# Performance work log

Hardware: AMD Instinct MI355X
Metric: run time of the kernel (lower is better)

Reference implementation:

```python
import jax, jax.numpy as jnp
import numpy as np

TH = 1.0            # q_threshold for all IF neurons
POS_MAX = 7.0       # level//2 - 1, level=16, sym=True
NEG_MIN = -8.0      # -(level//2)
PREFIRE = 0.2       # attn_softmax_IF.prefire
S_QUANT = 7.0       # spiking_softmax scale = level//2 - 1
NUM_HEADS = 8


def if_step(x, vmem0, acc0, th=TH, pos_max=POS_MAX, neg_min=NEG_MIN):
    """One timestep of a symmetric ST-BIF neuron with straight-through surrogate.
    Forward: spike in {-1,0,+1}*th gated by membrane and accumulator saturation.
    Backward: identity (STE), accumulator is a constant."""
    acc0f = acc0.astype(x.dtype)
    v = vmem0 + x
    pos = jnp.logical_and(v >= th, acc0f < pos_max)
    neg = jnp.logical_and(v < 0.0, acc0f > neg_min)
    spike = pos.astype(x.dtype) - neg.astype(x.dtype)
    out_hard = spike * th
    out = x + jax.lax.stop_gradient(out_hard - x)  # STE: fwd=spike*th, bwd=identity
    acc = jax.lax.stop_gradient(acc0f + spike)     # running spike count (constant wrt grads)
    return out, acc


def setup_inputs() -> dict:
    key = jax.random.key(0)
    ks = jax.random.split(key, 16)
    B, N, C, H = 4, 1024, 512, NUM_HEADS
    D = C // H
    f32 = jnp.float32
    inp = {
        "x": jax.random.normal(ks[0], (B, N, C), dtype=f32),
        "w_qkv": jax.random.normal(ks[1], (3 * C, C), dtype=f32) * 0.02,
        "b_qkv": jnp.zeros((3 * C,), dtype=f32),
        "w_proj": jax.random.normal(ks[2], (C, C), dtype=f32) * 0.02,
        "b_proj": jnp.zeros((C,), dtype=f32),
        "q_vmem": jax.random.uniform(ks[3], (B, H, N, D), dtype=f32),
        "k_vmem": jax.random.uniform(ks[4], (B, H, N, D), dtype=f32),
        "v_vmem": jax.random.uniform(ks[5], (B, H, N, D), dtype=f32),
        "attn_vmem": jax.random.uniform(ks[6], (B, H, N, N), dtype=f32),
        "q_acc0": jax.random.randint(ks[7], (B, H, N, D), 0, 8).astype(jnp.int32),
        "k_acc0": jax.random.randint(ks[8], (B, H, N, D), 0, 8).astype(jnp.int32),
        "v_acc0": jax.random.randint(ks[9], (B, H, N, D), 0, 8).astype(jnp.int32),
        "attn_acc0": jax.random.randint(ks[10], (B, H, N, N), 0, 8).astype(jnp.int32),
    }
    return inp


def reference(x, w_qkv, b_qkv, w_proj, b_proj,
              q_vmem, k_vmem, v_vmem, attn_vmem,
              q_acc0, k_acc0, v_acc0, attn_acc0):
    B, N, C = x.shape
    H = NUM_HEADS
    D = C // H
    scale = D ** -0.5
    sg = jax.lax.stop_gradient

    # qkv projection -> [3, B, H, N, D]
    qkv = (x @ w_qkv.T + b_qkv).reshape(B, N, 3, H, D).transpose(2, 0, 3, 1, 4)
    q_in, k_in, v_in = qkv[0], qkv[1], qkv[2]

    # ST-BIF IF neurons (one timestep, carried state)
    q_s, q_acc = if_step(q_in, q_vmem, q_acc0)
    k_s, k_acc = if_step(k_in, k_vmem, k_acc0)
    v_s, v_acc = if_step(v_in, v_vmem, v_acc0)

    q = q_s * scale
    # accumulator corrections: acc_q * q_threshold (*scale for q) minus detached spike output
    q_corr = sg(q_acc * TH * scale - q)
    k_corr = sg(k_acc * TH - k_s)
    v_corr = sg(v_acc * TH - v_s)

    # multi: (q + q_corr) @ k^T + q @ k_corr^T   -> [B, H, N, N]
    attn = (jnp.einsum('bhnd,bhmd->bhnm', q + q_corr, k_s)
            + jnp.einsum('bhnd,bhmd->bhnm', q, k_corr))

    # spiking softmax substitute: softmax of the (accumulated) scores, scaled to quant range
    attn = jax.nn.softmax(attn, axis=-1) * S_QUANT

    # attn_softmax_IF with prefire bias on the membrane
    attn_s, attn_acc = if_step(attn, attn_vmem + PREFIRE * TH, attn_acc0)
    attn_corr = sg(attn_acc * TH - attn_s)

    # multi1: (attn + attn_corr) @ v + attn @ v_corr  -> [B, H, N, D]
    out = (jnp.einsum('bhnm,bhmd->bhnd', attn_s + attn_corr, v_s)
           + jnp.einsum('bhnm,bhmd->bhnd', attn_s, v_corr))

    # after_attn_IF: fresh state (rounding init 0.5*th, zero accumulator)
    out, _ = if_step(out, jnp.asarray(0.5 * TH, out.dtype), jnp.zeros_like(out))

    out = out.transpose(0, 2, 1, 3).reshape(B, N, C)
    return out @ w_proj.T + b_proj
```

## Files before the change

kernel.cpp:

```cpp
#include <hip/hip_runtime.h>
#include <hip/hip_bf16.h>
#include <cstdint>

typedef short short8 __attribute__((ext_vector_type(8)));
typedef float f32x4 __attribute__((ext_vector_type(4)));
typedef int   int4v __attribute__((ext_vector_type(4)));
typedef _Float16 fp16x8 __attribute__((ext_vector_type(8)));

using bf16 = __hip_bfloat16;

#define MFMA16(a, b, c) __builtin_amdgcn_mfma_f32_16x16x32_bf16((a), (b), (c), 0, 0, 0)
#define MFMAI8(a, b, c) __builtin_amdgcn_mfma_i32_16x16x64_i8((a), (b), (c), 0, 0, 0)
#define MFMAF16(a, b, c) __builtin_amdgcn_mfma_f32_16x16x32_f16((a), (b), (c), 0, 0, 0)

__device__ __forceinline__ short8 ldb8(const bf16* p) {
    return *reinterpret_cast<const short8*>(p);
}

__global__ __launch_bounds__(256) void k_prep(
    const float* __restrict__ X, const float* __restrict__ W, const float* __restrict__ Wp,
    _Float16* __restrict__ Xh, _Float16* __restrict__ Xl,
    _Float16* __restrict__ Wh, _Float16* __restrict__ Wl, bf16* __restrict__ Wpb)
{
    const int NX = 4096 * 512, NW = 1536 * 512, NP = 512 * 512;
    for (int i = blockIdx.x * 256 + threadIdx.x; i < NX + NW + NP; i += gridDim.x * 256) {
        if (i < NX) {
            const float v = X[i] * 512.0f;
            const _Float16 h = (_Float16)v;
            Xh[i] = h;
            Xl[i] = (_Float16)((v - (float)h) * 2048.0f);
        } else if (i < NX + NW) {
            const int j = i - NX;
            const float v = W[j] * 512.0f;
            const _Float16 h = (_Float16)v;
            Wh[j] = h;
            Wl[j] = (_Float16)((v - (float)h) * 2048.0f);
        } else {
            const int j = i - NX - NW;
            Wpb[j] = __float2bfloat16(Wp[j]);
        }
    }
}

__global__ __launch_bounds__(256, 3) void k_qkv_f16(
    const _Float16* __restrict__ Xh, const _Float16* __restrict__ Xl,
    const _Float16* __restrict__ Wh, const _Float16* __restrict__ Wl,
    const float* __restrict__ bq,
    const float* __restrict__ qvm, const float* __restrict__ kvm, const float* __restrict__ vvm,
    const int* __restrict__ qac, const int* __restrict__ kac, const int* __restrict__ vac,
    int8_t* __restrict__ Q2, int8_t* __restrict__ K2c,
    int8_t* __restrict__ VsT, int8_t* __restrict__ VaT)
{
    const int tid = threadIdx.x;
    const int w = tid >> 6, lane = tid & 63, lo = lane & 15, hi = lane >> 4;
    const int wr = w >> 1, wc = w & 1;
    const int r0 = blockIdx.y * 64 + wr * 32;
    const int c0 = blockIdx.x * 128 + wc * 64;

    f32x4 hh[2][4] = {};
    f32x4 md[2][4] = {};

    const _Float16* xhp = Xh + (size_t)(r0 + lo) * 512 + hi * 8;
    const _Float16* xlp = Xl + (size_t)(r0 + lo) * 512 + hi * 8;
    const _Float16* whp = Wh + (size_t)(c0 + lo) * 512 + hi * 8;
    const _Float16* wlp = Wl + (size_t)(c0 + lo) * 512 + hi * 8;

    for (int kc = 0; kc < 16; ++kc) {
        const int ko = kc * 32;
        const fp16x8 Ah0 = *reinterpret_cast<const fp16x8*>(xhp + ko);
        const fp16x8 Ah1 = *reinterpret_cast<const fp16x8*>(xhp + ko + 16 * 512);
        const fp16x8 Al0 = *reinterpret_cast<const fp16x8*>(xlp + ko);
        const fp16x8 Al1 = *reinterpret_cast<const fp16x8*>(xlp + ko + 16 * 512);
        fp16x8 Bh[4], Bl[4];
        #pragma unroll
        for (int j = 0; j < 4; ++j) {
            Bh[j] = *reinterpret_cast<const fp16x8*>(whp + ko + j * 16 * 512);
            Bl[j] = *reinterpret_cast<const fp16x8*>(wlp + ko + j * 16 * 512);
        }
        #pragma unroll
        for (int j = 0; j < 4; ++j) {
            hh[0][j] = MFMAF16(Ah0, Bh[j], hh[0][j]);
            hh[1][j] = MFMAF16(Ah1, Bh[j], hh[1][j]);
            md[0][j] = MFMAF16(Ah0, Bl[j], md[0][j]);
            md[0][j] = MFMAF16(Al0, Bh[j], md[0][j]);
            md[1][j] = MFMAF16(Ah1, Bl[j], md[1][j]);
            md[1][j] = MFMAF16(Al1, Bh[j], md[1][j]);
        }
    }

    const int sel = (unsigned)c0 >> 9;
    const float* VM = (sel == 0) ? qvm : (sel == 1) ? kvm : vvm;
    const int*   AC = (sel == 0) ? qac : (sel == 1) ? kac : vac;

    #pragma unroll
    for (int i = 0; i < 2; ++i) {
        const int rowb = r0 + i * 16 + hi * 4;
        const int b = rowb >> 10, nb = rowb & 1023;
        #pragma unroll
        for (int j = 0; j < 4; ++j) {
            const int c = c0 + j * 16 + lo;
            const int ch = c & 511;
            const int hh_ = ch >> 6, d = ch & 63;
            const int bh = b * 8 + hh_;
            const float bcol = bq[c];
            int sp[4], a4[4];
            #pragma unroll
            for (int r = 0; r < 4; ++r) {
                const size_t gi = (size_t)(bh * 1024 + nb + r) * 64 + d;
                const float vm = VM[gi];
                const int a0 = AC[gi];
                const float val = fmaf(md[i][j][r], 0x1p-11f, hh[i][j][r]) * 0x1p-18f;
                const float v_ = vm + (val + bcol);
                int s = ((v_ >= 1.0f) && (a0 < 7)) ? 1 : 0;
                if (v_ < 0.0f) s -= 1;
                sp[r] = s; a4[r] = a0;
            }
            if (sel == 2) {
                uchar4 us, ua;
                us.x = (uint8_t)sp[0]; us.y = (uint8_t)sp[1]; us.z = (uint8_t)sp[2]; us.w = (uint8_t)sp[3];
                ua.x = (uint8_t)a4[0]; ua.y = (uint8_t)a4[1]; ua.z = (uint8_t)a4[2]; ua.w = (uint8_t)a4[3];
                const size_t vi = (size_t)(bh * 64 + d) * 1024 + nb;
                *reinterpret_cast<uchar4*>(VsT + vi) = us;
                *reinterpret_cast<uchar4*>(VaT + vi) = ua;
            } else {
                int8_t* base = ((sel == 0) ? Q2 : K2c) + (size_t)(bh * 1024 + nb) * 128 + d;
                #pragma unroll
                for (int r = 0; r < 4; ++r) {
                    const int v0 = (sel == 0) ? a4[r] + sp[r] : sp[r];
                    const int v1 = (sel == 0) ? sp[r]         : a4[r];
                    base[r * 128]      = (int8_t)v0;
                    base[r * 128 + 64] = (int8_t)v1;
                }
            }
        }
    }
}

__global__ __launch_bounds__(256, 4) void k_attn(
    const int8_t* __restrict__ Q2, const int8_t* __restrict__ K2c,
    const float* __restrict__ avm, const int* __restrict__ aac,
    const int8_t* __restrict__ VsT, const int8_t* __restrict__ VaT,
    bf16* __restrict__ O2)
{
    __shared__ alignas(16) char Sc[33280];
    int*   const maxb = (int*)(Sc + 32768);
    float* const sumb = (float*)(Sc + 33024);
    const int w = threadIdx.x >> 6, lane = threadIdx.x & 63;
    const int lo = lane & 15, hi = lane >> 4;
    const int bh = blockIdx.z * 8 + blockIdx.y;
    const int n0 = blockIdx.x * 16;

    int4v sc[16];
    {
        const int8_t* qb = Q2 + ((size_t)(bh * 1024 + n0 + lo)) * 128 + hi * 16;
        const int4v qa0 = *reinterpret_cast<const int4v*>(qb);
        const int4v qa1 = *reinterpret_cast<const int4v*>(qb + 64);
        const int8_t* kbp = K2c + ((size_t)(bh * 1024 + w * 256 + lo)) * 128 + hi * 16;
        int4v b0[2], b1[2];
        b0[0] = *reinterpret_cast<const int4v*>(kbp);
        b1[0] = *reinterpret_cast<const int4v*>(kbp + 64);
        b0[1] = *reinterpret_cast<const int4v*>(kbp + 2048);
        b1[1] = *reinterpret_cast<const int4v*>(kbp + 2048 + 64);
        #pragma unroll
        for (int t = 0; t < 16; ++t) {
            const int4v c0f = b0[t & 1], c1f = b1[t & 1];
            if (t < 14) {
                const int8_t* np = kbp + (t + 2) * 2048;
                b0[t & 1] = *reinterpret_cast<const int4v*>(np);
                b1[t & 1] = *reinterpret_cast<const int4v*>(np + 64);
            }
            int4v s = {0, 0, 0, 0};
            s = MFMAI8(c0f, qa0, s);
            s = MFMAI8(c1f, qa1, s);
            sc[t] = s;
        }
    }

    const float* vmp = avm + ((size_t)(bh * 1024 + n0 + lo)) * 1024 + w * 256 + hi * 4;
    const int*   acp = aac + ((size_t)(bh * 1024 + n0 + lo)) * 1024 + w * 256 + hi * 4;
    float4 vmr[4]; int4 acr[4];
    #pragma unroll
    for (int j = 0; j < 4; ++j) {
        vmr[j] = *reinterpret_cast<const float4*>(vmp + j * 16);
        acr[j] = *reinterpret_cast<const int4*>(acp + j * 16);
    }

    int mxi = sc[0][0];
    #pragma unroll
    for (int t = 0; t < 16; ++t)
        #pragma unroll
        for (int r = 0; r < 4; ++r)
            mxi = max(mxi, sc[t][r]);
    mxi = max(mxi, __shfl_xor(mxi, 16));
    mxi = max(mxi, __shfl_xor(mxi, 32));
    if (lane < 16) maxb[w * 16 + lo] = mxi;
    __syncthreads();
    const int M = max(max(maxb[lo], maxb[16 + lo]), max(maxb[32 + lo], maxb[48 + lo]));

    const float kls = 0.18033688011112042f;
    float sum = 0.f;
    #pragma unroll
    for (int t = 0; t < 16; ++t)
        #pragma unroll
        for (int r = 0; r < 4; ++r)
            sum += exp2f(kls * (float)(sc[t][r] - M));
    sum += __shfl_xor(sum, 16);
    sum += __shfl_xor(sum, 32);
    if (lane < 16) sumb[w * 16 + lo] = sum;
    __syncthreads();
    const float Stot = (sumb[lo] + sumb[16 + lo]) + (sumb[32 + lo] + sumb[48 + lo]);
    const float rsum = 7.0f / Stot;

    #pragma unroll
    for (int t = 0; t < 16; ++t) {
        const float4 vmc = vmr[t & 3];
        const int4  acc_ = acr[t & 3];
        if (t < 12) {
            vmr[t & 3] = *reinterpret_cast<const float4*>(vmp + (t + 4) * 16);
            acr[t & 3] = *reinterpret_cast<const int4*>(acp + (t + 4) * 16);
        }
        const float vr[4] = {vmc.x, vmc.y, vmc.z, vmc.w};
        const int   ar[4] = {acc_.x, acc_.y, acc_.z, acc_.w};
        unsigned b1v[4], b2v[4];
        #pragma unroll
        for (int i = 0; i < 4; ++i) {
            const float e_ = exp2f(kls * (float)(sc[t][i] - M));
            const float p7 = e_ * rsum;
            const float v_ = (vr[i] + 0.2f) + p7;
            const int a0i = ar[i];
            const int sp = ((v_ >= 1.0f) && (a0i < 7)) ? 1 : 0;
            b1v[i] = (unsigned)(a0i + sp);
            b2v[i] = (unsigned)sp;
        }
        const unsigned p1u = b1v[0] | (b1v[1] << 8) | (b1v[2] << 16) | (b1v[3] << 24);
        const unsigned p2u = b2v[0] | (b2v[1] << 8) | (b2v[2] << 16) | (b2v[3] << 24);
        char* pb = Sc + lo * 1024 + ((w * 256 + t * 16 + hi * 4) ^ ((lo & 7) << 4));
        *reinterpret_cast<unsigned*>(pb)         = p1u;
        *reinterpret_cast<unsigned*>(pb + 16384) = p2u;
    }
    __syncthreads();

    {
        const int d0 = w * 16;
        const int8_t* vs = VsT + ((size_t)(bh * 64 + d0 + lo)) * 1024 + hi * 16;
        const int8_t* va = VaT + ((size_t)(bh * 64 + d0 + lo)) * 1024 + hi * 16;
        int4v nvs = *reinterpret_cast<const int4v*>(vs);
        int4v nva = *reinterpret_cast<const int4v*>(va);
        int4v acc = {0, 0, 0, 0};
        for (int tt = 0; tt < 16; ++tt) {
            const int4v cvs = nvs, cva = nva;
            if (tt < 15) {
                nvs = *reinterpret_cast<const int4v*>(vs + (tt + 1) * 64);
                nva = *reinterpret_cast<const int4v*>(va + (tt + 1) * 64);
            }
            const char* pb = Sc + lo * 1024 + ((tt * 64 + hi * 16) ^ ((lo & 7) << 4));
            const int4v a1 = *reinterpret_cast<const int4v*>(pb);
            const int4v a2 = *reinterpret_cast<const int4v*>(pb + 16384);
            acc = MFMAI8(a1, cvs, acc);
            acc = MFMAI8(a2, cva, acc);
        }
        #pragma unroll
        for (int r = 0; r < 4; ++r) {
            const int n = n0 + hi * 4 + r;
            const float o = (float)acc[r];
            const float o2 = (o >= 0.5f ? 1.f : 0.f) - (o < -0.5f ? 1.f : 0.f);
            O2[((size_t)(blockIdx.z * 1024 + n)) * 512 + blockIdx.y * 64 + d0 + lo] = __float2bfloat16(o2);
        }
    }
}

__global__ __launch_bounds__(256) void k_proj(
    const bf16* __restrict__ O2, const bf16* __restrict__ W, const float* __restrict__ bias,
    float* __restrict__ Y)
{
    const int w = threadIdx.x >> 6, lane = threadIdx.x & 63;
    const int lo = lane & 15, hi = lane >> 4;
    const int r0 = blockIdx.y * 16;
    const int c0 = blockIdx.x * 256 + w * 64;

    f32x4 acc[4] = {{0.f,0.f,0.f,0.f},{0.f,0.f,0.f,0.f},{0.f,0.f,0.f,0.f},{0.f,0.f,0.f,0.f}};
    const bf16* op = O2 + (size_t)(r0 + lo) * 512 + hi * 8;
    #pragma unroll 4
    for (int kb = 0; kb < 16; ++kb) {
        short8 a = ldb8(op + kb * 32);
        #pragma unroll
        for (int t = 0; t < 4; ++t) {
            short8 b = ldb8(W + (size_t)(c0 + t * 16 + lo) * 512 + kb * 32 + hi * 8);
            acc[t] = MFMA16(a, b, acc[t]);
        }
    }
    #pragma unroll
    for (int t = 0; t < 4; ++t) {
        const int col = c0 + t * 16 + lo;
        const float bcol = bias[col];
        #pragma unroll
        for (int r = 0; r < 4; ++r) {
            const int rr = r0 + hi * 4 + r;
            Y[(size_t)rr * 512 + col] = acc[t][r] + bcol;
        }
    }
}

extern "C" void kernel_launch(void* const* d_in, const int* in_sizes, int n_in,
                              void* d_out, int out_size, void* d_ws, size_t ws_size,
                              hipStream_t stream)
{
    const float* x     = (const float*)d_in[0];
    const float* wqkv  = (const float*)d_in[1];
    const float* bqkv  = (const float*)d_in[2];
    const float* wproj = (const float*)d_in[3];
    const float* bproj = (const float*)d_in[4];
    const float* qvm   = (const float*)d_in[5];
    const float* kvm   = (const float*)d_in[6];
    const float* vvm   = (const float*)d_in[7];
    const float* avm   = (const float*)d_in[8];
    const int*   qac   = (const int*)d_in[9];
    const int*   kac   = (const int*)d_in[10];
    const int*   vac   = (const int*)d_in[11];
    const int*   aac   = (const int*)d_in[12];

    char* p = (char*)d_ws;
    int8_t*   Q2  = (int8_t*)p;   p += (size_t)32 * 1024 * 128;
    int8_t*   K2c = (int8_t*)p;   p += (size_t)32 * 1024 * 128;
    int8_t*   VsT = (int8_t*)p;   p += (size_t)32 * 64 * 1024;
    int8_t*   VaT = (int8_t*)p;   p += (size_t)32 * 64 * 1024;
    bf16*     O2  = (bf16*)p;     p += (size_t)4096 * 512 * 2;
    bf16*     Wpb = (bf16*)p;     p += (size_t)512 * 512 * 2;
    _Float16* Xh  = (_Float16*)p; p += (size_t)4096 * 512 * 2;
    _Float16* Xl  = (_Float16*)p; p += (size_t)4096 * 512 * 2;
    _Float16* Wh  = (_Float16*)p; p += (size_t)1536 * 512 * 2;
    _Float16* Wl  = (_Float16*)p; p += (size_t)1536 * 512 * 2;

    k_prep<<<dim3(2048), 256, 0, stream>>>(x, wqkv, wproj, Xh, Xl, Wh, Wl, Wpb);
    k_qkv_f16<<<dim3(12, 64), 256, 0, stream>>>(Xh, Xl, Wh, Wl, bqkv, qvm, kvm, vvm,
                                                qac, kac, vac, Q2, K2c, VsT, VaT);
    k_attn<<<dim3(64, 8, 4), 256, 0, stream>>>(Q2, K2c, avm, aac, VsT, VaT, O2);
    k_proj<<<dim3(2, 256), 256, 0, stream>>>(O2, Wpb, bproj, (float*)d_out);
}
```

Before: 463.8 us.

## Precompute accumulator-by-V product and merge spike V operands in attention

```diff
diff --git a/kernel.cpp b/kernel.cpp
--- a/kernel.cpp
+++ b/kernel.cpp
@@ -16,6 +16,8 @@
 __device__ __forceinline__ short8 ldb8(const bf16* p) {
     return *reinterpret_cast<const short8*>(p);
 }
+__device__ __forceinline__ int lo16(unsigned u) { return (int)(u << 16) >> 16; }
+__device__ __forceinline__ int hi16(unsigned u) { return (int)u >> 16; }
 
 __global__ __launch_bounds__(256) void k_prep(
     const float* __restrict__ X, const float* __restrict__ W, const float* __restrict__ Wp,
@@ -118,7 +120,8 @@
             if (sel == 2) {
                 uchar4 us, ua;
                 us.x = (uint8_t)sp[0]; us.y = (uint8_t)sp[1]; us.z = (uint8_t)sp[2]; us.w = (uint8_t)sp[3];
-                ua.x = (uint8_t)a4[0]; ua.y = (uint8_t)a4[1]; ua.z = (uint8_t)a4[2]; ua.w = (uint8_t)a4[3];
+                ua.x = (uint8_t)(a4[0] + sp[0]); ua.y = (uint8_t)(a4[1] + sp[1]);
+                ua.z = (uint8_t)(a4[2] + sp[2]); ua.w = (uint8_t)(a4[3] + sp[3]);
                 const size_t vi = (size_t)(bh * 64 + d) * 1024 + nb;
                 *reinterpret_cast<uchar4*>(VsT + vi) = us;
                 *reinterpret_cast<uchar4*>(VaT + vi) = ua;
@@ -136,25 +139,76 @@
     }
 }
 
+__global__ __launch_bounds__(256, 2) void k_av0(
+    const int* __restrict__ aac, const int8_t* __restrict__ VsT,
+    uint8_t* __restrict__ aac8, int* __restrict__ AV0)
+{
+    const int w = threadIdx.x >> 6, lane = threadIdx.x & 63;
+    const int lo = lane & 15, hi = lane >> 4;
+    const int bh = blockIdx.y;
+    const int row = blockIdx.x * 64 + w * 16 + lo;
+    const size_t arow = ((size_t)bh * 1024 + row) * 1024;
+
+    int4 buf[2][4];
+    {
+        const int4* ap0 = reinterpret_cast<const int4*>(aac + arow + hi * 16);
+        const int4* ap1 = reinterpret_cast<const int4*>(aac + arow + 64 + hi * 16);
+        #pragma unroll
+        for (int j = 0; j < 4; ++j) { buf[0][j] = ap0[j]; buf[1][j] = ap1[j]; }
+    }
+
+    int4v acc[4] = {{0,0,0,0},{0,0,0,0},{0,0,0,0},{0,0,0,0}};
+    #pragma unroll
+    for (int tt = 0; tt < 16; ++tt) {
+        int4 c[4];
+        #pragma unroll
+        for (int j = 0; j < 4; ++j) c[j] = buf[tt & 1][j];
+        if (tt < 14) {
+            const int4* ap = reinterpret_cast<const int4*>(aac + arow + (tt + 2) * 64 + hi * 16);
+            #pragma unroll
+            for (int j = 0; j < 4; ++j) buf[tt & 1][j] = ap[j];
+        }
+        int4v af;
+        af[0] = (int)(unsigned)(c[0].x | (c[0].y << 8) | (c[0].z << 16) | (c[0].w << 24));
+        af[1] = (int)(unsigned)(c[1].x | (c[1].y << 8) | (c[1].z << 16) | (c[1].w << 24));
+        af[2] = (int)(unsigned)(c[2].x | (c[2].y << 8) | (c[2].z << 16) | (c[2].w << 24));
+        af[3] = (int)(unsigned)(c[3].x | (c[3].y << 8) | (c[3].z << 16) | (c[3].w << 24));
+        *reinterpret_cast<int4v*>(aac8 + arow + tt * 64 + hi * 16) = af;
+        #pragma unroll
+        for (int dt = 0; dt < 4; ++dt) {
+            const int4v bf = *reinterpret_cast<const int4v*>(
+                VsT + ((size_t)(bh * 64 + dt * 16 + lo)) * 1024 + tt * 64 + hi * 16);
+            acc[dt] = MFMAI8(af, bf, acc[dt]);
+        }
+    }
+    #pragma unroll
+    for (int dt = 0; dt < 4; ++dt)
+        #pragma unroll
+        for (int r = 0; r < 4; ++r)
+            AV0[((size_t)bh * 1024 + blockIdx.x * 64 + w * 16 + hi * 4 + r) * 64 + dt * 16 + lo] = acc[dt][r];
+}
+
 __global__ __launch_bounds__(256, 4) void k_attn(
     const int8_t* __restrict__ Q2, const int8_t* __restrict__ K2c,
-    const float* __restrict__ avm, const int* __restrict__ aac,
-    const int8_t* __restrict__ VsT, const int8_t* __restrict__ VaT,
+    const float* __restrict__ avm, const uint8_t* __restrict__ aac8,
+    const int8_t* __restrict__ Vsum, const int* __restrict__ AV0,
     bf16* __restrict__ O2)
 {
-    __shared__ alignas(16) char Sc[33280];
+    __shared__ alignas(16) char Sc[33792];
     int*   const maxb = (int*)(Sc + 32768);
-    float* const sumb = (float*)(Sc + 33024);
+    float* const sumb = (float*)(Sc + 33280);
     const int w = threadIdx.x >> 6, lane = threadIdx.x & 63;
     const int lo = lane & 15, hi = lane >> 4;
     const int bh = blockIdx.z * 8 + blockIdx.y;
-    const int n0 = blockIdx.x * 16;
-
-    int4v sc[16];
+    const int n0 = blockIdx.x * 32;
+
+    unsigned pA[16][2], pB[16][2];
     {
         const int8_t* qb = Q2 + ((size_t)(bh * 1024 + n0 + lo)) * 128 + hi * 16;
-        const int4v qa0 = *reinterpret_cast<const int4v*>(qb);
-        const int4v qa1 = *reinterpret_cast<const int4v*>(qb + 64);
+        const int4v qA0 = *reinterpret_cast<const int4v*>(qb);
+        const int4v qA1 = *reinterpret_cast<const int4v*>(qb + 64);
+        const int4v qB0 = *reinterpret_cast<const int4v*>(qb + 16 * 128);
+        const int4v qB1 = *reinterpret_cast<const int4v*>(qb + 16 * 128 + 64);
         const int8_t* kbp = K2c + ((size_t)(bh * 1024 + w * 256 + lo)) * 128 + hi * 16;
         int4v b0[2], b1[2];
         b0[0] = *reinterpret_cast<const int4v*>(kbp);
@@ -169,102 +223,121 @@
                 b0[t & 1] = *reinterpret_cast<const int4v*>(np);
                 b1[t & 1] = *reinterpret_cast<const int4v*>(np + 64);
             }
-            int4v s = {0, 0, 0, 0};
-            s = MFMAI8(c0f, qa0, s);
-            s = MFMAI8(c1f, qa1, s);
-            sc[t] = s;
-        }
-    }
-
-    const float* vmp = avm + ((size_t)(bh * 1024 + n0 + lo)) * 1024 + w * 256 + hi * 4;
-    const int*   acp = aac + ((size_t)(bh * 1024 + n0 + lo)) * 1024 + w * 256 + hi * 4;
-    float4 vmr[4]; int4 acr[4];
-    #pragma unroll
-    for (int j = 0; j < 4; ++j) {
-        vmr[j] = *reinterpret_cast<const float4*>(vmp + j * 16);
-        acr[j] = *reinterpret_cast<const int4*>(acp + j * 16);
-    }
-
-    int mxi = sc[0][0];
-    #pragma unroll
-    for (int t = 0; t < 16; ++t)
-        #pragma unroll
-        for (int r = 0; r < 4; ++r)
-            mxi = max(mxi, sc[t][r]);
-    mxi = max(mxi, __shfl_xor(mxi, 16));
-    mxi = max(mxi, __shfl_xor(mxi, 32));
-    if (lane < 16) maxb[w * 16 + lo] = mxi;
+            int4v sA = {0, 0, 0, 0}, sB = {0, 0, 0, 0};
+            sA = MFMAI8(c0f, qA0, sA); sA = MFMAI8(c1f, qA1, sA);
+            sB = MFMAI8(c0f, qB0, sB); sB = MFMAI8(c1f, qB1, sB);
+            pA[t][0] = (sA[0] & 0xFFFF) | ((unsigned)sA[1] << 16);
+            pA[t][1] = (sA[2] & 0xFFFF) | ((unsigned)sA[3] << 16);
+            pB[t][0] = (sB[0] & 0xFFFF) | ((unsigned)sB[1] << 16);
+            pB[t][1] = (sB[2] & 0xFFFF) | ((unsigned)sB[3] << 16);
+        }
+    }
+
+    const float*   vmpA = avm  + ((size_t)(bh * 1024 + n0 + lo)) * 1024 + w * 256 + hi * 4;
+    const float*   vmpB = vmpA + (size_t)16 * 1024;
+    const uint8_t* acpA = aac8 + ((size_t)(bh * 1024 + n0 + lo)) * 1024 + w * 256 + hi * 4;
+    const uint8_t* acpB = acpA + (size_t)16 * 1024;
+    float4 vmr[8]; uchar4 acr[8];
+#define PF(u) { vmr[(u)&7] = *reinterpret_cast<const float4*>((u) < 16 ? vmpA + (u)*16 : vmpB + ((u)-16)*16); \
+                acr[(u)&7] = *reinterpret_cast<const uchar4*>((u) < 16 ? acpA + (u)*16 : acpB + ((u)-16)*16); }
+    PF(0) PF(1) PF(2) PF(3) PF(4) PF(5) PF(6) PF(7)
+
+    int mxA = -32768, mxB = -32768;
+    #pragma unroll
+    for (int t = 0; t < 16; ++t) {
+        mxA = max(mxA, max(max(lo16(pA[t][0]), hi16(pA[t][0])), max(lo16(pA[t][1]), hi16(pA[t][1]))));
+        mxB = max(mxB, max(max(lo16(pB[t][0]), hi16(pB[t][0])), max(lo16(pB[t][1]), hi16(pB[t][1]))));
+    }
+    mxA = max(mxA, __shfl_xor(mxA, 16)); mxA = max(mxA, __shfl_xor(mxA, 32));
+    mxB = max(mxB, __shfl_xor(mxB, 16)); mxB = max(mxB, __shfl_xor(mxB, 32));
+    if (lane < 16) { maxb[w * 16 + lo] = mxA; maxb[64 + w * 16 + lo] = mxB; }
     __syncthreads();
-    const int M = max(max(maxb[lo], maxb[16 + lo]), max(maxb[32 + lo], maxb[48 + lo]));
+    const int MA = max(max(maxb[lo], maxb[16 + lo]), max(maxb[32 + lo], maxb[48 + lo]));
+    const int MB = max(max(maxb[64 + lo], maxb[80 + lo]), max(maxb[96 + lo], maxb[112 + lo]));
 
     const float kls = 0.18033688011112042f;
-    float sum = 0.f;
-    #pragma unroll
-    for (int t = 0; t < 16; ++t)
-        #pragma unroll
-        for (int r = 0; r < 4; ++r)
-            sum += exp2f(kls * (float)(sc[t][r] - M));
-    sum += __shfl_xor(sum, 16);
-    sum += __shfl_xor(sum, 32);
-    if (lane < 16) sumb[w * 16 + lo] = sum;
+    float sA = 0.f, sB = 0.f;
+    #pragma unroll
+    for (int t = 0; t < 16; ++t) {
+        sA += exp2f(kls * (float)(lo16(pA[t][0]) - MA));
+        sA += exp2f(kls * (float)(hi16(pA[t][0]) - MA));
+        sA += exp2f(kls * (float)(lo16(pA[t][1]) - MA));
+        sA += exp2f(kls * (float)(hi16(pA[t][1]) - MA));
+        sB += exp2f(kls * (float)(lo16(pB[t][0]) - MB));
+        sB += exp2f(kls * (float)(hi16(pB[t][0]) - MB));
+        sB += exp2f(kls * (float)(lo16(pB[t][1]) - MB));
+        sB += exp2f(kls * (float)(hi16(pB[t][1]) - MB));
+    }
+    sA += __shfl_xor(sA, 16); sA += __shfl_xor(sA, 32);
+    sB += __shfl_xor(sB, 16); sB += __shfl_xor(sB, 32);
+    if (lane < 16) { sumb[w * 16 + lo] = sA; sumb[64 + w * 16 + lo] = sB; }
     __syncthreads();
-    const float Stot = (sumb[lo] + sumb[16 + lo]) + (sumb[32 + lo] + sumb[48 + lo]);
-    const float rsum = 7.0f / Stot;
-
-    #pragma unroll
-    for (int t = 0; t < 16; ++t) {
-        const float4 vmc = vmr[t & 3];
-        const int4  acc_ = acr[t & 3];
-        if (t < 12) {
-            vmr[t & 3] = *reinterpret_cast<const float4*>(vmp + (t + 4) * 16);
-            acr[t & 3] = *reinterpret_cast<const int4*>(acp + (t + 4) * 16);
-        }
-        const float vr[4] = {vmc.x, vmc.y, vmc.z, vmc.w};
-        const int   ar[4] = {acc_.x, acc_.y, acc_.z, acc_.w};
-        unsigned b1v[4], b2v[4];
+    const float rsA = 7.0f / ((sumb[lo] + sumb[16 + lo]) + (sumb[32 + lo] + sumb[48 + lo]));
+    const float rsB = 7.0f / ((sumb[64 + lo] + sumb[80 + lo]) + (sumb[96 + lo] + sumb[112 + lo]));
+
+    #pragma unroll
+    for (int u = 0; u < 32; ++u) {
+        const float4 vm = vmr[u & 7];
+        const uchar4 a8 = acr[u & 7];
+        if (u < 24) PF(u + 8)
+        const int t = u & 15;
+        const unsigned s0 = (u < 16) ? pA[t][0] : pB[t][0];
+        const unsigned s1 = (u < 16) ? pA[t][1] : pB[t][1];
+        const int   Mi = (u < 16) ? MA : MB;
+        const float rs = (u < 16) ? rsA : rsB;
+        const int sv[4] = { lo16(s0), hi16(s0), lo16(s1), hi16(s1) };
+        const float vr[4] = { vm.x, vm.y, vm.z, vm.w };
+        const int   ar[4] = { a8.x, a8.y, a8.z, a8.w };
+        unsigned pk = 0;
         #pragma unroll
         for (int i = 0; i < 4; ++i) {
-            const float e_ = exp2f(kls * (float)(sc[t][i] - M));
-            const float p7 = e_ * rsum;
+            const float e_ = exp2f(kls * (float)(sv[i] - Mi));
+            const float p7 = e_ * rs;
             const float v_ = (vr[i] + 0.2f) + p7;
-            const int a0i = ar[i];
-            const int sp = ((v_ >= 1.0f) && (a0i < 7)) ? 1 : 0;
-            b1v[i] = (unsigned)(a0i + sp);
-            b2v[i] = (unsigned)sp;
-        }
-        const unsigned p1u = b1v[0] | (b1v[1] << 8) | (b1v[2] << 16) | (b1v[3] << 24);
-        const unsigned p2u = b2v[0] | (b2v[1] << 8) | (b2v[2] << 16) | (b2v[3] << 24);
-        char* pb = Sc + lo * 1024 + ((w * 256 + t * 16 + hi * 4) ^ ((lo & 7) << 4));
-        *reinterpret_cast<unsigned*>(pb)         = p1u;
-        *reinterpret_cast<unsigned*>(pb + 16384) = p2u;
-    }
+            const unsigned sp = ((v_ >= 1.0f) && (ar[i] < 7)) ? 1u : 0u;
+            pk |= sp << (8 * i);
+        }
+        const int row = lo + ((u < 16) ? 0 : 16);
+        char* pb = Sc + row * 1024 + ((w * 256 + t * 16 + hi * 4) ^ ((row & 7) << 4));
+        *reinterpret_cast<unsigned*>(pb) = pk;
+    }
+#undef PF
     __syncthreads();
 
     {
         const int d0 = w * 16;
-        const int8_t* vs = VsT + ((size_t)(bh * 64 + d0 + lo)) * 1024 + hi * 16;
-        const int8_t* va = VaT + ((size_t)(bh * 64 + d0 + lo)) * 1024 + hi * 16;
-        int4v nvs = *reinterpret_cast<const int4v*>(vs);
-        int4v nva = *reinterpret_cast<const int4v*>(va);
-        int4v acc = {0, 0, 0, 0};
+        const int* avp = AV0 + ((size_t)(bh * 1024 + n0 + hi * 4)) * 64 + d0 + lo;
+        int avA[4], avB[4];
+        #pragma unroll
+        for (int r = 0; r < 4; ++r) { avA[r] = avp[(size_t)r * 64]; avB[r] = avp[(size_t)(16 + r) * 64]; }
+
+        const int8_t* vp = Vsum + ((size_t)(bh * 64 + d0 + lo)) * 1024 + hi * 16;
+        int4v nv0 = *reinterpret_cast<const int4v*>(vp);
+        int4v nv1 = *reinterpret_cast<const int4v*>(vp + 64);
+        int4v accA = {0, 0, 0, 0}, accB = {0, 0, 0, 0};
+        #pragma unroll
         for (int tt = 0; tt < 16; ++tt) {
-            const int4v cvs = nvs, cva = nva;
-            if (tt < 15) {
-                nvs = *reinterpret_cast<const int4v*>(vs + (tt + 1) * 64);
-                nva = *reinterpret_cast<const int4v*>(va + (tt + 1) * 64);
+            const int4v cv = (tt & 1) ? nv1 : nv0;
+            if (tt < 14) {
+                if (tt & 1) nv1 = *reinterpret_cast<const int4v*>(vp + (tt + 2) * 64);
+                else        nv0 = *reinterpret_cast<const int4v*>(vp + (tt + 2) * 64);
             }
-            const char* pb = Sc + lo * 1024 + ((tt * 64 + hi * 16) ^ ((lo & 7) << 4));
-            const int4v a1 = *reinterpret_cast<const int4v*>(pb);
-            const int4v a2 = *reinterpret_cast<const int4v*>(pb + 16384);
-            acc = MFMAI8(a1, cvs, acc);
-            acc = MFMAI8(a2, cva, acc);
+            const int ko = tt * 64 + hi * 16;
+            const int4v a1 = *reinterpret_cast<const int4v*>(Sc + lo * 1024 + (ko ^ ((lo & 7) << 4)));
+            const int4v a2 = *reinterpret_cast<const int4v*>(Sc + (lo + 16) * 1024 + (ko ^ ((lo & 7) << 4)));
+            accA = MFMAI8(a1, cv, accA);
+            accB = MFMAI8(a2, cv, accB);
         }
         #pragma unroll
         for (int r = 0; r < 4; ++r) {
-            const int n = n0 + hi * 4 + r;
-            const float o = (float)acc[r];
-            const float o2 = (o >= 0.5f ? 1.f : 0.f) - (o < -0.5f ? 1.f : 0.f);
-            O2[((size_t)(blockIdx.z * 1024 + n)) * 512 + blockIdx.y * 64 + d0 + lo] = __float2bfloat16(o2);
+            const int oA = accA[r] + avA[r];
+            const int oB = accB[r] + avB[r];
+            const float fA = (float)oA, fB = (float)oB;
+            const float o2A = (fA >= 0.5f ? 1.f : 0.f) - (fA < -0.5f ? 1.f : 0.f);
+            const float o2B = (fB >= 0.5f ? 1.f : 0.f) - (fB < -0.5f ? 1.f : 0.f);
+            const int nA = n0 + hi * 4 + r;
+            O2[((size_t)(blockIdx.z * 1024 + nA)) * 512 + blockIdx.y * 64 + d0 + lo] = __float2bfloat16(o2A);
+            O2[((size_t)(blockIdx.z * 1024 + nA + 16)) * 512 + blockIdx.y * 64 + d0 + lo] = __float2bfloat16(o2B);
         }
     }
 }
@@ -320,20 +393,23 @@
     const int*   aac   = (const int*)d_in[12];
 
     char* p = (char*)d_ws;
-    int8_t*   Q2  = (int8_t*)p;   p += (size_t)32 * 1024 * 128;
-    int8_t*   K2c = (int8_t*)p;   p += (size_t)32 * 1024 * 128;
-    int8_t*   VsT = (int8_t*)p;   p += (size_t)32 * 64 * 1024;
-    int8_t*   VaT = (int8_t*)p;   p += (size_t)32 * 64 * 1024;
-    bf16*     O2  = (bf16*)p;     p += (size_t)4096 * 512 * 2;
-    bf16*     Wpb = (bf16*)p;     p += (size_t)512 * 512 * 2;
-    _Float16* Xh  = (_Float16*)p; p += (size_t)4096 * 512 * 2;
-    _Float16* Xl  = (_Float16*)p; p += (size_t)4096 * 512 * 2;
-    _Float16* Wh  = (_Float16*)p; p += (size_t)1536 * 512 * 2;
-    _Float16* Wl  = (_Float16*)p; p += (size_t)1536 * 512 * 2;
+    int8_t*   Q2   = (int8_t*)p;   p += (size_t)32 * 1024 * 128;
+    int8_t*   K2c  = (int8_t*)p;   p += (size_t)32 * 1024 * 128;
+    int8_t*   VsT  = (int8_t*)p;   p += (size_t)32 * 64 * 1024;
+    int8_t*   VaT  = (int8_t*)p;   p += (size_t)32 * 64 * 1024;
+    bf16*     O2   = (bf16*)p;     p += (size_t)4096 * 512 * 2;
+    bf16*     Wpb  = (bf16*)p;     p += (size_t)512 * 512 * 2;
+    _Float16* Xh   = (_Float16*)p; p += (size_t)4096 * 512 * 2;
+    _Float16* Xl   = (_Float16*)p; p += (size_t)4096 * 512 * 2;
+    _Float16* Wh   = (_Float16*)p; p += (size_t)1536 * 512 * 2;
+    _Float16* Wl   = (_Float16*)p; p += (size_t)1536 * 512 * 2;
+    uint8_t*  aac8 = (uint8_t*)p;  p += (size_t)32 * 1024 * 1024;
+    int*      AV0  = (int*)p;      p += (size_t)32 * 1024 * 64 * 4;
 
     k_prep<<<dim3(2048), 256, 0, stream>>>(x, wqkv, wproj, Xh, Xl, Wh, Wl, Wpb);
     k_qkv_f16<<<dim3(12, 64), 256, 0, stream>>>(Xh, Xl, Wh, Wl, bqkv, qvm, kvm, vvm,
                                                 qac, kac, vac, Q2, K2c, VsT, VaT);
-    k_attn<<<dim3(64, 8, 4), 256, 0, stream>>>(Q2, K2c, avm, aac, VsT, VaT, O2);
+    k_av0<<<dim3(16, 32), 256, 0, stream>>>(aac, VsT, aac8, AV0);
+    k_attn<<<dim3(32, 8, 4), 256, 0, stream>>>(Q2, K2c, avm, aac8, VaT, AV0, O2);
     k_proj<<<dim3(2, 256), 256, 0, stream>>>(O2, Wpb, bproj, (float*)d_out);
 }
```

Result: slower. 582.0 us (+25.5%).
